# Optimization experiments

Hardware: AMD Instinct MI355X
Metric: run time of the kernel (lower is better)

Reference implementation:

```python
import jax, jax.numpy as jnp
import numpy as np

N, E, D, H = 10000, 160000, 128, 8


def setup_inputs() -> dict:
    key = jax.random.key(0)
    ks = jax.random.split(key, 12)
    s = 0.05  # xavier-ish init scale
    return {
        "x": jax.random.normal(ks[0], (N, D), jnp.float32),
        "conn_ex": jax.random.normal(ks[1], (E, D), jnp.float32),
        "edge_index": jax.random.randint(ks[2], (2, E), 0, N),
        "sqrt_deg": jax.random.uniform(ks[3], (N, 1), jnp.float32, 0.5, 2.0),
        "qkv_w": (jax.random.normal(ks[4], (3 * D, D)) * s).astype(jnp.float32),
        "qkv_b": jnp.zeros((3 * D,), jnp.float32),
        "w1": (jax.random.normal(ks[5], (2 * D, D)) * s).astype(jnp.float32),
        "b1": jnp.zeros((2 * D,), jnp.float32),
        "wscore": (jax.random.normal(ks[6], (D // H, H, 1)) * s).astype(jnp.float32),
        "w2": (jax.random.normal(ks[7], (D, D)) * s).astype(jnp.float32),
        "b2": jnp.zeros((D,), jnp.float32),
        "bn_c_g": jnp.ones((D,), jnp.float32),
        "bn_c_b": jnp.zeros((D,), jnp.float32),
        "deg_coef": (jax.random.normal(ks[8], (1, D, 2)) * s).astype(jnp.float32),
        "ffn1_w": (jax.random.normal(ks[9], (2 * D, D)) * s).astype(jnp.float32),
        "ffn1_b": jnp.zeros((2 * D,), jnp.float32),
        "ffn2_w": (jax.random.normal(ks[10], (D, 2 * D)) * s).astype(jnp.float32),
        "ffn2_b": jnp.zeros((D,), jnp.float32),
        "bn1_g": jnp.ones((D,), jnp.float32),
        "bn1_b": jnp.zeros((D,), jnp.float32),
        "bn2_g": jnp.ones((D,), jnp.float32),
        "bn2_b": jnp.zeros((D,), jnp.float32),
        "num_nodes": N,
    }


def _bn(v, g, b):
    # BatchNorm1d, training-mode statistics (biased variance), eps=1e-5
    mu = v.mean(0)
    var = v.var(0)
    return (v - mu) / jnp.sqrt(var + 1e-5) * g + b


def _seg_softmax(s, idx, n):
    # sparse softmax over segments of dim 0 given by idx (pyg_softmax)
    m = jax.ops.segment_max(s, idx, num_segments=n)
    e = jnp.exp(s - m[idx])
    den = jax.ops.segment_sum(e, idx, num_segments=n)[idx] + 1e-16
    return e / den


def reference(x, conn_ex, edge_index, sqrt_deg, qkv_w, qkv_b, w1, b1, wscore,
              w2, b2, bn_c_g, bn_c_b, deg_coef, ffn1_w, ffn1_b, ffn2_w, ffn2_b,
              bn1_g, bn1_b, bn2_g, bn2_b, num_nodes):
    n, d = x.shape
    h = wscore.shape[1]
    dh = d // h
    # packed QKV projection
    qkv = x @ qkv_w.T + qkv_b
    Q, K, V = qkv[:, :d], qkv[:, d:2 * d], qkv[:, 2 * d:]
    dst, src = edge_index[0], edge_index[1]
    e = dst.shape[0]
    # edge-conditioned weights/bias: conn_lin1 output split into (Ew, Eb)
    Eh = conn_ex @ w1.T + b1  # [E, 2d]
    Ew, Eb = Eh[:, :d], Eh[:, d:]
    c = (Q[dst] + K[src]) * Ew
    # sqrt(relu(c)) - sqrt(relu(-c)) == sign(c)*sqrt(|c|) (signed sqrt)
    c = jnp.sign(c) * jnp.sqrt(jnp.abs(c)) + Eb
    c = jax.nn.relu(c)  # act; dropout p=0
    c2 = jax.nn.relu(_bn(c @ w2.T + b2 + conn_ex, bn_c_g, bn_c_b))  # [E, d]
    # attention scores per head
    score = jnp.einsum('ehd,dhc->ehc', c.reshape(e, h, dh), wscore)  # [E,H,1]
    score = jnp.clip(score, -5.0, 5.0)
    alpha = _seg_softmax(score, dst, num_nodes)  # [E,H,1]
    # scatter-add aggregation of weighted V and conn features
    nagg = jax.ops.segment_sum(V[src].reshape(e, h, dh) * alpha, dst, num_segments=num_nodes)
    cagg = jax.ops.segment_sum(c2.reshape(e, h, dh) * alpha, dst, num_segments=num_nodes)
    nh = (nagg + cagg).reshape(n, d)
    # degree rescaling
    nh = (jnp.stack([nh, nh * sqrt_deg], axis=-1) * deg_coef).sum(-1)
    h_res = nh + x
    nh = _bn(h_res, bn1_g, bn1_b)
    nh = jax.nn.relu(nh @ ffn1_w.T + ffn1_b) @ ffn2_w.T + ffn2_b
    nh = _bn(nh + h_res, bn2_g, bn2_b)
    return nh, c2
```

## Files before the change

### kernel.cpp

```cpp
#include <hip/hip_runtime.h>
#include <math.h>

typedef float f4 __attribute__((ext_vector_type(4)));
typedef float f2 __attribute__((ext_vector_type(2)));
typedef short bf16x8 __attribute__((ext_vector_type(8)));
typedef float f32x4v __attribute__((ext_vector_type(4)));
typedef unsigned short u16x4 __attribute__((ext_vector_type(4)));

#define N_NODES 10000
#define N_EDGES 160000

#define OFF_DEN     0
#define OFF_SUMS    80000
#define OFF_DEG     80768
#define ZERO_WORDS  90768
#define OFF_ROWPTR  90768
#define OFF_CURSOR  100772
#define OFF_ELIST   110772
#define OFF_SS      270772
#define OFF_WBF     271544
#define OFF_QKV     353464
#define OFF_ESC     4193464
#define OFF_HRES    5473464
#define OFF_MID     6753464
#define OFF_CONNB   9313464

__device__ __forceinline__ unsigned short f2bf(float f) {
  unsigned int u = __float_as_uint(f);
  u = (u + 0x7fffu + ((u >> 16) & 1u)) >> 16;
  return (unsigned short)u;
}
__device__ __forceinline__ float bf2f(unsigned short p) {
  return __uint_as_float(((unsigned int)p) << 16);
}

__global__ void k_prep(const float* __restrict__ conn, const float* __restrict__ w1,
                       const float* __restrict__ w2, const float* __restrict__ qw,
                       const float* __restrict__ f1w, const float* __restrict__ f2w,
                       const int* __restrict__ ei, unsigned short* __restrict__ connB,
                       unsigned short* __restrict__ wb16, int* __restrict__ deg) {
  int g = blockIdx.x * 256 + threadIdx.x;
  if (g < 2560000) {
    int i0 = g * 8;
    f4 a = *(const f4*)&conn[i0];
    f4 b = *(const f4*)&conn[i0 + 4];
    u16x4 pa = { f2bf(a[0]), f2bf(a[1]), f2bf(a[2]), f2bf(a[3]) };
    u16x4 pb = { f2bf(b[0]), f2bf(b[1]), f2bf(b[2]), f2bf(b[3]) };
    *(u16x4*)&connB[i0] = pa;
    *(u16x4*)&connB[i0 + 4] = pb;
  }
  if (g < 20480) {
    int i0 = g * 8;
    const float* src; unsigned short* dst; int off;
    if (i0 < 32768)       { src = w1;  dst = wb16;          off = i0; }
    else if (i0 < 49152)  { src = w2;  dst = wb16 + 32768;  off = i0 - 32768; }
    else if (i0 < 98304)  { src = qw;  dst = wb16 + 49152;  off = i0 - 49152; }
    else if (i0 < 131072) { src = f1w; dst = wb16 + 98304;  off = i0 - 98304; }
    else                  { src = f2w; dst = wb16 + 131072; off = i0 - 131072; }
    f4 a = *(const f4*)&src[off];
    f4 b = *(const f4*)&src[off + 4];
    u16x4 pa = { f2bf(a[0]), f2bf(a[1]), f2bf(a[2]), f2bf(a[3]) };
    u16x4 pb = { f2bf(b[0]), f2bf(b[1]), f2bf(b[2]), f2bf(b[3]) };
    *(u16x4*)&dst[off] = pa;
    *(u16x4*)&dst[off + 4] = pb;
  }
  if (g < N_EDGES) atomicAdd(&deg[ei[g]], 1);
}

__global__ __launch_bounds__(512, 6) void k_edge(
    const unsigned short* __restrict__ connB, const int* __restrict__ ei,
    const float* __restrict__ qkv, const unsigned short* __restrict__ w1bf,
    const unsigned short* __restrict__ w2bf, const float* __restrict__ b1,
    const float* __restrict__ b2, const float* __restrict__ wsc_g,
    float* __restrict__ t_out, float* __restrict__ escore,
    float* __restrict__ den, float* __restrict__ bnc_sums) {
  __shared__ unsigned short qkcBF[8192];
  __shared__ float csum[128], csq[128];
  const int tid = threadIdx.x;
  const int e0 = blockIdx.x * 64;
  if (tid < 128) csum[tid] = 0.f;
  else if (tid < 256) csq[tid - 128] = 0.f;

#pragma unroll
  for (int it = 0; it < 4; ++it) {
    int i = tid + it * 512;
    int row = i >> 5, kq = i & 31;
    int dst = ei[e0 + row], src = ei[N_EDGES + e0 + row];
    f4 qv = *(const f4*)&qkv[dst * 384 + kq * 4];
    f4 kv = *(const f4*)&qkv[src * 384 + 128 + kq * 4];
    f4 s = qv + kv;
    u16x4 sp = { f2bf(s[0]), f2bf(s[1]), f2bf(s[2]), f2bf(s[3]) };
    int wb = ((row * 256 + kq * 8) ^ ((row & 7) << 4)) >> 1;
    *(u16x4*)&qkcBF[wb] = sp;
  }

  const int w = tid >> 6;
  const int lq = (tid >> 4) & 3;
  const int lr = tid & 15;

  f32x4v accW[4] = {}, accB[4] = {};
#pragma unroll
  for (int ks = 0; ks < 4; ++ks) {
    bf16x8 bW = *(const bf16x8*)&w1bf[(w * 16 + lr) * 128 + ks * 32 + lq * 8];
    bf16x8 bB = *(const bf16x8*)&w1bf[(128 + w * 16 + lr) * 128 + ks * 32 + lq * 8];
#pragma unroll
    for (int rf = 0; rf < 4; ++rf) {
      bf16x8 a = *(const bf16x8*)&connB[(e0 + rf * 16 + lr) * 128 + ks * 32 + lq * 8];
      accW[rf] = __builtin_amdgcn_mfma_f32_16x16x32_bf16(a, bW, accW[rf], 0, 0, 0);
      accB[rf] = __builtin_amdgcn_mfma_f32_16x16x32_bf16(a, bB, accB[rf], 0, 0, 0);
    }
  }
  __syncthreads();

  {
    const float wv = wsc_g[lr * 8 + w];
    const float bw = b1[w * 16 + lr];
    const float bb = b1[128 + w * 16 + lr];
#pragma unroll
    for (int rf = 0; rf < 4; ++rf) {
#pragma unroll
      for (int r = 0; r < 4; ++r) {
        int row = rf * 16 + lq * 4 + r;
        int qoff = ((row * 256 + (w * 16 + lr) * 2) ^ ((row & 7) << 4)) >> 1;
        float qk = bf2f(qkcBF[qoff]);
        float ew = accW[rf][r] + bw;
        float eb = accB[rf][r] + bb;
        float z = qk * ew;
        float cval = fmaxf(copysignf(sqrtf(fabsf(z)), z) + eb, 0.f);
        float sp = cval * wv;
        sp += __shfl_xor(sp, 1);
        sp += __shfl_xor(sp, 2);
        sp += __shfl_xor(sp, 4);
        sp += __shfl_xor(sp, 8);
        if (lr == 0) {
          float s = fminf(fmaxf(sp, -5.f), 5.f);
          float es = expf(s);
          escore[(e0 + row) * 8 + w] = es;
          atomicAdd(&den[ei[e0 + row] * 8 + w], es);
        }
        qkcBF[qoff] = f2bf(cval);
      }
    }
  }
  __syncthreads();

  const int r16 = (w & 3) * 16;
  const int cb = (w >> 2) * 64;
  f32x4v acc2[4] = {};
#pragma unroll
  for (int ks = 0; ks < 4; ++ks) {
    int row = r16 + lr;
    int off = ((row * 256 + ks * 64 + lq * 16) ^ ((row & 7) << 4)) >> 1;
    bf16x8 a = *(const bf16x8*)&qkcBF[off];
#pragma unroll
    for (int cf = 0; cf < 4; ++cf) {
      bf16x8 b = *(const bf16x8*)&w2bf[(cb + cf * 16 + lr) * 128 + ks * 32 + lq * 8];
      acc2[cf] = __builtin_amdgcn_mfma_f32_16x16x32_bf16(a, b, acc2[cf], 0, 0, 0);
    }
  }
#pragma unroll
  for (int cf = 0; cf < 4; ++cf) {
    const int col = cb + cf * 16 + lr;
    const float bias = b2[col];
    float sp = 0.f, qp = 0.f;
#pragma unroll
    for (int r = 0; r < 4; ++r) {
      int row = r16 + lq * 4 + r;
      float cn = bf2f(connB[(e0 + row) * 128 + col]);
      float t = acc2[cf][r] + bias + cn;
      t_out[(e0 + row) * 128 + col] = t;
      sp += t;
      qp += t * t;
    }
    sp += __shfl_xor(sp, 16);
    sp += __shfl_xor(sp, 32);
    qp += __shfl_xor(qp, 16);
    qp += __shfl_xor(qp, 32);
    if (lq == 0) {
      atomicAdd(&csum[col], sp);
      atomicAdd(&csq[col], qp);
    }
  }
  __syncthreads();
  if (tid < 128) {
    atomicAdd(&bnc_sums[tid], csum[tid]);
    atomicAdd(&bnc_sums[128 + tid], csq[tid]);
  }
}

__global__ __launch_bounds__(256, 6) void k_qkv(const float* __restrict__ x,
                                                const unsigned short* __restrict__ qwbf,
                                                const float* __restrict__ b,
                                                float* __restrict__ out) {
  __shared__ unsigned short xBF[4096];
  const int tid = threadIdx.x;
  const int r0 = blockIdx.x * 32;
#pragma unroll
  for (int it = 0; it < 4; ++it) {
    int i = tid + it * 256;
    int row = i >> 5, kq = i & 31;
    int gr = r0 + row; if (gr > N_NODES - 1) gr = N_NODES - 1;
    f4 v = *(const f4*)&x[gr * 128 + kq * 4];
    u16x4 p = { f2bf(v[0]), f2bf(v[1]), f2bf(v[2]), f2bf(v[3]) };
    int wb = ((row * 256 + kq * 8) ^ ((row & 7) << 4)) >> 1;
    *(u16x4*)&xBF[wb] = p;
  }
  __syncthreads();
  const int w = tid >> 6, lq = (tid >> 4) & 3, lr = tid & 15;
  f32x4v acc[2][6] = {};
#pragma unroll
  for (int ks = 0; ks < 4; ++ks) {
    bf16x8 a0, a1;
    {
      int row = lr;
      a0 = *(const bf16x8*)&xBF[((row * 256 + ks * 64 + lq * 16) ^ ((row & 7) << 4)) >> 1];
      row = 16 + lr;
      a1 = *(const bf16x8*)&xBF[((row * 256 + ks * 64 + lq * 16) ^ ((row & 7) << 4)) >> 1];
    }
#pragma unroll
    for (int cf = 0; cf < 6; ++cf) {
      bf16x8 bv = *(const bf16x8*)&qwbf[(w * 96 + cf * 16 + lr) * 128 + ks * 32 + lq * 8];
      acc[0][cf] = __builtin_amdgcn_mfma_f32_16x16x32_bf16(a0, bv, acc[0][cf], 0, 0, 0);
      acc[1][cf] = __builtin_amdgcn_mfma_f32_16x16x32_bf16(a1, bv, acc[1][cf], 0, 0, 0);
    }
  }
#pragma unroll
  for (int rf = 0; rf < 2; ++rf) {
#pragma unroll
    for (int cf = 0; cf < 6; ++cf) {
      int col = w * 96 + cf * 16 + lr;
      float bias = b[col];
#pragma unroll
      for (int r = 0; r < 4; ++r) {
        int gr = r0 + rf * 16 + lq * 4 + r;
        if (gr < N_NODES) out[gr * 384 + col] = acc[rf][cf][r] + bias;
      }
    }
  }
}

__global__ __launch_bounds__(1024) void k_scanfin(
    const int* __restrict__ deg, int* __restrict__ rowptr, int* __restrict__ cursor,
    const float* __restrict__ sums, const float* __restrict__ g,
    const float* __restrict__ bta, float* __restrict__ ss) {
  if (blockIdx.x == 1) {
    int c = threadIdx.x;
    if (c < 128) {
      float inv_n = 1.f / N_EDGES;
      float mu = sums[c] * inv_n;
      float var = sums[128 + c] * inv_n - mu * mu;
      float sc = g[c] / sqrtf(var + 1e-5f);
      ss[c] = sc;
      ss[128 + c] = bta[c] - mu * sc;
    }
    return;
  }
  __shared__ int wsum[16];
  const int t = threadIdx.x;
  const int base = t * 10;
  int d[10];
  int s0 = 0;
#pragma unroll
  for (int i = 0; i < 10; ++i) {
    int idx = base + i;
    d[i] = (idx < N_NODES) ? deg[idx] : 0;
    s0 += d[i];
  }
  int s = s0;
  const int lane = t & 63;
#pragma unroll
  for (int o = 1; o < 64; o <<= 1) {
    int v = __shfl_up(s, o);
    if (lane >= o) s += v;
  }
  if (lane == 63) wsum[t >> 6] = s;
  __syncthreads();
  if (t < 16) {
    int v = wsum[t];
#pragma unroll
    for (int o = 1; o < 16; o <<= 1) {
      int u = __shfl_up(v, o);
      if (t >= o) v += u;
    }
    wsum[t] = v;
  }
  __syncthreads();
  int incl = s + ((t >= 64) ? wsum[(t >> 6) - 1] : 0);
  int run = incl - s0;
#pragma unroll
  for (int i = 0; i < 10; ++i) {
    int idx = base + i;
    if (idx < N_NODES) {
      rowptr[idx] = run;
      cursor[idx] = run;
      run += d[i];
    }
  }
  if (t == 1023) rowptr[N_NODES] = incl;
}

__global__ void k_scatter(const int* __restrict__ ei, int* __restrict__ cursor,
                          int* __restrict__ elist) {
  int e = blockIdx.x * 256 + threadIdx.x;
  if (e < N_EDGES) {
    int pos = atomicAdd(&cursor[ei[e]], 1);
    elist[pos] = e;
  }
}

__global__ void k_bnfin(const float* __restrict__ sums, const float* __restrict__ g,
                        const float* __restrict__ bta, float inv_n,
                        float* __restrict__ ss) {
  int c = threadIdx.x;
  float mu = sums[c] * inv_n;
  float var = sums[128 + c] * inv_n - mu * mu;
  float sc = g[c] / sqrtf(var + 1e-5f);
  ss[c] = sc;
  ss[128 + c] = bta[c] - mu * sc;
}

__global__ __launch_bounds__(256) void k_agg(
    const int* __restrict__ rowptr, const int* __restrict__ elist,
    const int* __restrict__ ei, const float* __restrict__ escore,
    const float* __restrict__ den, float* __restrict__ t_c2,
    const float* __restrict__ qkv, const float* __restrict__ x,
    const float* __restrict__ sqrtdeg, const float* __restrict__ degc,
    const float* __restrict__ ss, float* __restrict__ hres,
    float* __restrict__ bn1_sums) {
  __shared__ float csum[128], csq[128];
  const int tid = threadIdx.x;
  if (tid < 128) csum[tid] = 0.f;
  else csq[tid - 128] = 0.f;
  __syncthreads();
  const int sl = tid & 31;
  const int n = blockIdx.x * 8 + (tid >> 5);
  const int c0 = sl * 4;
  const int head = sl >> 2;
  const int st = rowptr[n], en = rowptr[n + 1];
  const float invd = 1.f / (den[n * 8 + head] + 1e-16f);
  const f4 sc = *(const f4*)&ss[c0];
  const f4 sh = *(const f4*)&ss[128 + c0];
  f4 acc = {};
  int e = (st < en) ? elist[st] : 0;
  for (int idx = st; idx < en; ++idx) {
    const int ec = e;
    if (idx + 1 < en) e = elist[idx + 1];
    const float al = escore[ec * 8 + head] * invd;
    const int src = ei[N_EDGES + ec];
    f4 tv = *(const f4*)&t_c2[ec * 128 + c0];
    f4 vv = *(const f4*)&qkv[src * 384 + 256 + c0];
    f4 c2v = tv * sc + sh;
#pragma unroll
    for (int t = 0; t < 4; ++t) c2v[t] = fmaxf(c2v[t], 0.f);
    *(f4*)&t_c2[ec * 128 + c0] = c2v;
    acc += al * (c2v + vv);
  }
  const float sd = sqrtdeg[n];
  f4 d0 = { degc[c0 * 2], degc[c0 * 2 + 2], degc[c0 * 2 + 4], degc[c0 * 2 + 6] };
  f4 d1 = { degc[c0 * 2 + 1], degc[c0 * 2 + 3], degc[c0 * 2 + 5], degc[c0 * 2 + 7] };
  f4 xr = *(const f4*)&x[n * 128 + c0];
  f4 hr = acc * (d0 + sd * d1) + xr;
  *(f4*)&hres[n * 128 + c0] = hr;
#pragma unroll
  for (int t = 0; t < 4; ++t) {
    atomicAdd(&csum[c0 + t], hr[t]);
    atomicAdd(&csq[c0 + t], hr[t] * hr[t]);
  }
  __syncthreads();
  if (tid < 128) {
    atomicAdd(&bn1_sums[tid], csum[tid]);
    atomicAdd(&bn1_sums[128 + tid], csq[tid]);
  }
}

__global__ __launch_bounds__(256, 6) void k_ffn1(const float* __restrict__ hres,
                                                 const float* __restrict__ ss,
                                                 const unsigned short* __restrict__ wbf,
                                                 const float* __restrict__ b,
                                                 float* __restrict__ mid) {
  __shared__ unsigned short aBF[4096];
  const int tid = threadIdx.x;
  const int r0 = blockIdx.x * 32;
#pragma unroll
  for (int it = 0; it < 4; ++it) {
    int i = tid + it * 256;
    int row = i >> 5, kq = i & 31;
    int gr = r0 + row; if (gr > N_NODES - 1) gr = N_NODES - 1;
    f4 v = *(const f4*)&hres[gr * 128 + kq * 4];
    f4 sc = *(const f4*)&ss[kq * 4];
    f4 sh = *(const f4*)&ss[128 + kq * 4];
    v = v * sc + sh;
    u16x4 p = { f2bf(v[0]), f2bf(v[1]), f2bf(v[2]), f2bf(v[3]) };
    int wb = ((row * 256 + kq * 8) ^ ((row & 7) << 4)) >> 1;
    *(u16x4*)&aBF[wb] = p;
  }
  __syncthreads();
  const int w = tid >> 6, lq = (tid >> 4) & 3, lr = tid & 15;
  f32x4v acc[2][4] = {};
#pragma unroll
  for (int ks = 0; ks < 4; ++ks) {
    bf16x8 a0, a1;
    {
      int row = lr;
      a0 = *(const bf16x8*)&aBF[((row * 256 + ks * 64 + lq * 16) ^ ((row & 7) << 4)) >> 1];
      row = 16 + lr;
      a1 = *(const bf16x8*)&aBF[((row * 256 + ks * 64 + lq * 16) ^ ((row & 7) << 4)) >> 1];
    }
#pragma unroll
    for (int cf = 0; cf < 4; ++cf) {
      bf16x8 bv = *(const bf16x8*)&wbf[(w * 64 + cf * 16 + lr) * 128 + ks * 32 + lq * 8];
      acc[0][cf] = __builtin_amdgcn_mfma_f32_16x16x32_bf16(a0, bv, acc[0][cf], 0, 0, 0);
      acc[1][cf] = __builtin_amdgcn_mfma_f32_16x16x32_bf16(a1, bv, acc[1][cf], 0, 0, 0);
    }
  }
#pragma unroll
  for (int rf = 0; rf < 2; ++rf) {
#pragma unroll
    for (int cf = 0; cf < 4; ++cf) {
      int col = w * 64 + cf * 16 + lr;
      float bias = b[col];
#pragma unroll
      for (int r = 0; r < 4; ++r) {
        int gr = r0 + rf * 16 + lq * 4 + r;
        if (gr < N_NODES) mid[gr * 256 + col] = fmaxf(acc[rf][cf][r] + bias, 0.f);
      }
    }
  }
}

__global__ __launch_bounds__(256, 6) void k_ffn2(const float* __restrict__ mid,
                                                 const unsigned short* __restrict__ wbf,
                                                 const float* __restrict__ b,
                                                 const float* __restrict__ hres,
                                                 float* __restrict__ y,
                                                 float* __restrict__ bn2_sums) {
  __shared__ unsigned short aBF[8192];
  __shared__ float csum[128], csq[128];
  const int tid = threadIdx.x;
  const int r0 = blockIdx.x * 32;
  if (tid < 128) csum[tid] = 0.f;
  else csq[tid - 128] = 0.f;
#pragma unroll
  for (int it = 0; it < 8; ++it) {
    int i = tid + it * 256;
    int row = i >> 6, kq = i & 63;
    int gr = r0 + row; if (gr > N_NODES - 1) gr = N_NODES - 1;
    f4 v = *(const f4*)&mid[gr * 256 + kq * 4];
    u16x4 p = { f2bf(v[0]), f2bf(v[1]), f2bf(v[2]), f2bf(v[3]) };
    int wb = ((row * 512 + kq * 8) ^ ((row & 7) << 4)) >> 1;
    *(u16x4*)&aBF[wb] = p;
  }
  __syncthreads();
  const int w = tid >> 6, lq = (tid >> 4) & 3, lr = tid & 15;
  f32x4v acc[2][2] = {};
#pragma unroll
  for (int ks = 0; ks < 8; ++ks) {
    bf16x8 a0, a1;
    {
      int row = lr;
      a0 = *(const bf16x8*)&aBF[((row * 512 + ks * 64 + lq * 16) ^ ((row & 7) << 4)) >> 1];
      row = 16 + lr;
      a1 = *(const bf16x8*)&aBF[((row * 512 + ks * 64 + lq * 16) ^ ((row & 7) << 4)) >> 1];
    }
#pragma unroll
    for (int cf = 0; cf < 2; ++cf) {
      bf16x8 bv = *(const bf16x8*)&wbf[(w * 32 + cf * 16 + lr) * 256 + ks * 32 + lq * 8];
      acc[0][cf] = __builtin_amdgcn_mfma_f32_16x16x32_bf16(a0, bv, acc[0][cf], 0, 0, 0);
      acc[1][cf] = __builtin_amdgcn_mfma_f32_16x16x32_bf16(a1, bv, acc[1][cf], 0, 0, 0);
    }
  }
#pragma unroll
  for (int rf = 0; rf < 2; ++rf) {
#pragma unroll
    for (int cf = 0; cf < 2; ++cf) {
      int col = w * 32 + cf * 16 + lr;
      float bias = b[col];
      float sp = 0.f, qp = 0.f;
#pragma unroll
      for (int r = 0; r < 4; ++r) {
        int gr = r0 + rf * 16 + lq * 4 + r;
        if (gr < N_NODES) {
          float o = acc[rf][cf][r] + bias + hres[gr * 128 + col];
          y[gr * 128 + col] = o;
          sp += o;
          qp += o * o;
        }
      }
      atomicAdd(&csum[col], sp);
      atomicAdd(&csq[col], qp);
    }
  }
  __syncthreads();
  if (tid < 128) {
    atomicAdd(&bn2_sums[tid], csum[tid]);
    atomicAdd(&bn2_sums[128 + tid], csq[tid]);
  }
}

__global__ void k_bnfinal(float* __restrict__ yio, const float* __restrict__ ss) {
  int i = blockIdx.x * 256 + threadIdx.x;
  if (i < N_NODES * 32) {
    int c = (i & 31) * 4;
    f4 v = *(const f4*)&yio[i * 4];
    f4 sc = *(const f4*)&ss[c];
    f4 sh = *(const f4*)&ss[128 + c];
    v = v * sc + sh;
    *(f4*)&yio[i * 4] = v;
  }
}

extern "C" void kernel_launch(void* const* d_in, const int* in_sizes, int n_in,
                              void* d_out, int out_size, void* d_ws, size_t ws_size,
                              hipStream_t stream) {
  const float* x      = (const float*)d_in[0];
  const float* conn   = (const float*)d_in[1];
  const int*   ei     = (const int*)d_in[2];
  const float* sqrtdg = (const float*)d_in[3];
  const float* qkv_w  = (const float*)d_in[4];
  const float* qkv_b  = (const float*)d_in[5];
  const float* w1     = (const float*)d_in[6];
  const float* b1     = (const float*)d_in[7];
  const float* wscore = (const float*)d_in[8];
  const float* w2     = (const float*)d_in[9];
  const float* b2     = (const float*)d_in[10];
  const float* bncg   = (const float*)d_in[11];
  const float* bncb   = (const float*)d_in[12];
  const float* degc   = (const float*)d_in[13];
  const float* f1w    = (const float*)d_in[14];
  const float* f1b    = (const float*)d_in[15];
  const float* f2w    = (const float*)d_in[16];
  const float* f2b    = (const float*)d_in[17];
  const float* bn1g   = (const float*)d_in[18];
  const float* bn1b   = (const float*)d_in[19];
  const float* bn2g   = (const float*)d_in[20];
  const float* bn2b   = (const float*)d_in[21];

  float* ws  = (float*)d_ws;
  int*   wsi = (int*)d_ws;
  float* outF = (float*)d_out;
  float* t_c2 = outF + N_NODES * 128;
  unsigned short* connB = (unsigned short*)(wsi + OFF_CONNB);
  unsigned short* wb16  = (unsigned short*)(wsi + OFF_WBF);
  unsigned short* w1bf  = wb16;
  unsigned short* w2bf  = wb16 + 32768;
  unsigned short* qwbf  = wb16 + 49152;
  unsigned short* f1wbf = wb16 + 98304;
  unsigned short* f2wbf = wb16 + 131072;

  (void)hipMemsetAsync(d_ws, 0, (size_t)ZERO_WORDS * 4, stream);

  k_prep<<<dim3(10000), dim3(256), 0, stream>>>(conn, w1, w2, qkv_w, f1w, f2w, ei,
                                                connB, wb16, wsi + OFF_DEG);
  k_qkv<<<dim3(313), dim3(256), 0, stream>>>(x, qwbf, qkv_b, ws + OFF_QKV);
  k_edge<<<dim3(2500), dim3(512), 0, stream>>>(connB, ei, ws + OFF_QKV, w1bf, w2bf,
                                               b1, b2, wscore, t_c2,
                                               ws + OFF_ESC, ws + OFF_DEN,
                                               ws + OFF_SUMS);
  k_scanfin<<<dim3(2), dim3(1024), 0, stream>>>(wsi + OFF_DEG, wsi + OFF_ROWPTR,
                                                wsi + OFF_CURSOR, ws + OFF_SUMS,
                                                bncg, bncb, ws + OFF_SS);
  k_scatter<<<dim3(625), dim3(256), 0, stream>>>(ei, wsi + OFF_CURSOR, wsi + OFF_ELIST);
  k_agg<<<dim3(1250), dim3(256), 0, stream>>>(wsi + OFF_ROWPTR, wsi + OFF_ELIST, ei,
                                              ws + OFF_ESC, ws + OFF_DEN, t_c2,
                                              ws + OFF_QKV, x, sqrtdg, degc,
                                              ws + OFF_SS, ws + OFF_HRES,
                                              ws + OFF_SUMS + 256);
  k_bnfin<<<dim3(1), dim3(128), 0, stream>>>(ws + OFF_SUMS + 256, bn1g, bn1b,
                                             1.f / N_NODES, ws + OFF_SS + 256);
  k_ffn1<<<dim3(313), dim3(256), 0, stream>>>(ws + OFF_HRES, ws + OFF_SS + 256,
                                              f1wbf, f1b, ws + OFF_MID);
  k_ffn2<<<dim3(313), dim3(256), 0, stream>>>(ws + OFF_MID, f2wbf, f2b, ws + OFF_HRES,
                                              outF, ws + OFF_SUMS + 512);
  k_bnfin<<<dim3(1), dim3(128), 0, stream>>>(ws + OFF_SUMS + 512, bn2g, bn2b,
                                             1.f / N_NODES, ws + OFF_SS + 512);
  k_bnfinal<<<dim3(1250), dim3(256), 0, stream>>>(outF, ws + OFF_SS + 512);
}
```

Before: 511.2 us.

## Fuse conn_ex bf16 conversion into edge kernel via swizzled LDS tile

Removes the separate pass in k_prep that converted the whole conn_ex tensor to bf16 in a global workspace. Each k_edge block now loads its 64-row fp32 conn tile once, converts it to bf16 into a swizzled shared-memory buffer, and reuses that buffer for both the lin1 MFMA A operand and the residual add. This drops a full write and re-read of the converted tensor plus the large prep launch, which shrinks to 625 blocks. In exchange it adds 16 KB of LDS per block, which may lower occupancy, and moves the barrier to before the first MFMA loop.

```diff
diff --git a/kernel.cpp b/kernel.cpp
--- a/kernel.cpp
+++ b/kernel.cpp
@@ -23,7 +23,6 @@
 #define OFF_ESC     4193464
 #define OFF_HRES    5473464
 #define OFF_MID     6753464
-#define OFF_CONNB   9313464
 
 __device__ __forceinline__ unsigned short f2bf(float f) {
   unsigned int u = __float_as_uint(f);
@@ -34,21 +33,11 @@
   return __uint_as_float(((unsigned int)p) << 16);
 }
 
-__global__ void k_prep(const float* __restrict__ conn, const float* __restrict__ w1,
-                       const float* __restrict__ w2, const float* __restrict__ qw,
-                       const float* __restrict__ f1w, const float* __restrict__ f2w,
-                       const int* __restrict__ ei, unsigned short* __restrict__ connB,
+__global__ void k_prep(const float* __restrict__ w1, const float* __restrict__ w2,
+                       const float* __restrict__ qw, const float* __restrict__ f1w,
+                       const float* __restrict__ f2w, const int* __restrict__ ei,
                        unsigned short* __restrict__ wb16, int* __restrict__ deg) {
   int g = blockIdx.x * 256 + threadIdx.x;
-  if (g < 2560000) {
-    int i0 = g * 8;
-    f4 a = *(const f4*)&conn[i0];
-    f4 b = *(const f4*)&conn[i0 + 4];
-    u16x4 pa = { f2bf(a[0]), f2bf(a[1]), f2bf(a[2]), f2bf(a[3]) };
-    u16x4 pb = { f2bf(b[0]), f2bf(b[1]), f2bf(b[2]), f2bf(b[3]) };
-    *(u16x4*)&connB[i0] = pa;
-    *(u16x4*)&connB[i0 + 4] = pb;
-  }
   if (g < 20480) {
     int i0 = g * 8;
     const float* src; unsigned short* dst; int off;
@@ -68,12 +57,13 @@
 }
 
 __global__ __launch_bounds__(512, 6) void k_edge(
-    const unsigned short* __restrict__ connB, const int* __restrict__ ei,
+    const float* __restrict__ conn, const int* __restrict__ ei,
     const float* __restrict__ qkv, const unsigned short* __restrict__ w1bf,
     const unsigned short* __restrict__ w2bf, const float* __restrict__ b1,
     const float* __restrict__ b2, const float* __restrict__ wsc_g,
     float* __restrict__ t_out, float* __restrict__ escore,
     float* __restrict__ den, float* __restrict__ bnc_sums) {
+  __shared__ unsigned short connBF[8192];
   __shared__ unsigned short qkcBF[8192];
   __shared__ float csum[128], csq[128];
   const int tid = threadIdx.x;
@@ -85,14 +75,18 @@
   for (int it = 0; it < 4; ++it) {
     int i = tid + it * 512;
     int row = i >> 5, kq = i & 31;
+    int wb = ((row * 256 + kq * 8) ^ ((row & 7) << 4)) >> 1;
+    f4 cv = *(const f4*)&conn[(e0 + row) * 128 + kq * 4];
+    u16x4 cp = { f2bf(cv[0]), f2bf(cv[1]), f2bf(cv[2]), f2bf(cv[3]) };
+    *(u16x4*)&connBF[wb] = cp;
     int dst = ei[e0 + row], src = ei[N_EDGES + e0 + row];
     f4 qv = *(const f4*)&qkv[dst * 384 + kq * 4];
     f4 kv = *(const f4*)&qkv[src * 384 + 128 + kq * 4];
     f4 s = qv + kv;
     u16x4 sp = { f2bf(s[0]), f2bf(s[1]), f2bf(s[2]), f2bf(s[3]) };
-    int wb = ((row * 256 + kq * 8) ^ ((row & 7) << 4)) >> 1;
     *(u16x4*)&qkcBF[wb] = sp;
   }
+  __syncthreads();
 
   const int w = tid >> 6;
   const int lq = (tid >> 4) & 3;
@@ -105,12 +99,13 @@
     bf16x8 bB = *(const bf16x8*)&w1bf[(128 + w * 16 + lr) * 128 + ks * 32 + lq * 8];
 #pragma unroll
     for (int rf = 0; rf < 4; ++rf) {
-      bf16x8 a = *(const bf16x8*)&connB[(e0 + rf * 16 + lr) * 128 + ks * 32 + lq * 8];
+      int row = rf * 16 + lr;
+      int off = ((row * 256 + ks * 64 + lq * 16) ^ ((row & 7) << 4)) >> 1;
+      bf16x8 a = *(const bf16x8*)&connBF[off];
       accW[rf] = __builtin_amdgcn_mfma_f32_16x16x32_bf16(a, bW, accW[rf], 0, 0, 0);
       accB[rf] = __builtin_amdgcn_mfma_f32_16x16x32_bf16(a, bB, accB[rf], 0, 0, 0);
     }
   }
-  __syncthreads();
 
   {
     const float wv = wsc_g[lr * 8 + w];
@@ -166,7 +161,8 @@
 #pragma unroll
     for (int r = 0; r < 4; ++r) {
       int row = r16 + lq * 4 + r;
-      float cn = bf2f(connB[(e0 + row) * 128 + col]);
+      int coff = ((row * 256 + col * 2) ^ ((row & 7) << 4)) >> 1;
+      float cn = bf2f(connBF[coff]);
       float t = acc2[cf][r] + bias + cn;
       t_out[(e0 + row) * 128 + col] = t;
       sp += t;
@@ -539,7 +535,6 @@
   int*   wsi = (int*)d_ws;
   float* outF = (float*)d_out;
   float* t_c2 = outF + N_NODES * 128;
-  unsigned short* connB = (unsigned short*)(wsi + OFF_CONNB);
   unsigned short* wb16  = (unsigned short*)(wsi + OFF_WBF);
   unsigned short* w1bf  = wb16;
   unsigned short* w2bf  = wb16 + 32768;
@@ -549,10 +544,10 @@
 
   (void)hipMemsetAsync(d_ws, 0, (size_t)ZERO_WORDS * 4, stream);
 
-  k_prep<<<dim3(10000), dim3(256), 0, stream>>>(conn, w1, w2, qkv_w, f1w, f2w, ei,
-                                                connB, wb16, wsi + OFF_DEG);
+  k_prep<<<dim3(625), dim3(256), 0, stream>>>(w1, w2, qkv_w, f1w, f2w, ei,
+                                              wb16, wsi + OFF_DEG);
   k_qkv<<<dim3(313), dim3(256), 0, stream>>>(x, qwbf, qkv_b, ws + OFF_QKV);
-  k_edge<<<dim3(2500), dim3(512), 0, stream>>>(connB, ei, ws + OFF_QKV, w1bf, w2bf,
+  k_edge<<<dim3(2500), dim3(512), 0, stream>>>(conn, ei, ws + OFF_QKV, w1bf, w2bf,
                                                b1, b2, wscore, t_c2,
                                                ws + OFF_ESC, ws + OFF_DEN,
                                                ws + OFF_SUMS);
```

After: 463.4 us. 9.4% less time.
